# Kernel tuning notes

Measured on AMD Instinct MI355X. Metric: run time of the kernel, lower is better.

## Reference

```python
import jax, jax.numpy as jnp
import numpy as np

B, L, C = 2, 2048, 2048
H, HKV, D = 16, 4, 128  # heads, kv heads, head_dim
G = H // HKV            # GQA group size
NEG = -1e9


def rms_norm(x, w, eps=1e-6):
    # FastRMSNorm: compute in fp32, scale by weight, cast back
    xf = x.astype(jnp.float32)
    y = xf * jax.lax.rsqrt(jnp.mean(xf * xf, axis=-1, keepdims=True) + eps) * w
    return y.astype(x.dtype)


def apply_rope(t, cos, sin):
    # t: (B, h, L, D); cos/sin: (L, D//2) broadcast to (1,1,L,D//2)
    t1, t2 = jnp.split(t, 2, axis=-1)
    c = cos[None, None]
    s = sin[None, None]
    return jnp.concatenate([t1 * c - t2 * s, t2 * c + t1 * s], axis=-1)


def setup_inputs() -> dict:
    key = jax.random.key(0)
    ks = jax.random.split(key, 8)
    x = jax.random.normal(ks[0], (B, L, C), jnp.float32)
    Wq = jax.random.normal(ks[1], (H * D, C), jnp.float32) * 0.02
    Wk = jax.random.normal(ks[2], (HKV * D, C), jnp.float32) * 0.02
    Wv = jax.random.normal(ks[3], (HKV * D, C), jnp.float32) * 0.02
    Wo = jax.random.normal(ks[4], (C, H * D), jnp.float32) * 0.02
    q_norm_w = jnp.ones((D,), jnp.float32)
    k_norm_w = jnp.ones((D,), jnp.float32)
    pos = jnp.arange(L, dtype=jnp.float32)[:, None]
    inv_freq = 1.0 / (10000.0 ** (jnp.arange(0, D, 2, dtype=jnp.float32) / D))
    ang = pos * inv_freq[None, :]            # (L, D//2)
    rope_cos = jnp.cos(ang)
    rope_sin = jnp.sin(ang)
    # VAR-style block-causal visibility: 8 blocks of 256, query block i sees key blocks <= i
    blk = jnp.arange(L) // 256
    vis = blk[None, :] <= blk[:, None]       # (L, L) bool
    attn_bias = jnp.where(vis, 0.0, NEG).astype(jnp.float32)[None, None]  # (1,1,L,L)
    return dict(x=x, Wq=Wq, Wk=Wk, Wv=Wv, Wo=Wo, q_norm_w=q_norm_w,
                k_norm_w=k_norm_w, rope_cos=rope_cos, rope_sin=rope_sin,
                attn_bias=attn_bias)


def reference(x, Wq, Wk, Wv, Wo, q_norm_w, k_norm_w, rope_cos, rope_sin, attn_bias):
    b, l, c = x.shape
    # fused projections -> (B, h, L, D)
    q = rms_norm((x @ Wq.T).reshape(b, l, H, D), q_norm_w).transpose(0, 2, 1, 3)
    k = rms_norm((x @ Wk.T).reshape(b, l, HKV, D), k_norm_w).transpose(0, 2, 1, 3)
    v = (x @ Wv.T).reshape(b, l, HKV, D).transpose(0, 2, 1, 3)
    q = apply_rope(q, rope_cos, rope_sin)
    k = apply_rope(k, rope_cos, rope_sin)
    scale = D ** -0.5
    # GQA: group query heads over kv heads
    qg = q.reshape(b, HKV, G, l, D)
    scores = jnp.einsum('bkgqd,bkKd->bkgqK', qg, k) * scale
    scores = scores + attn_bias[:, :, None]  # broadcast (1,1,1,L,L)
    probs = jax.nn.softmax(scores, axis=-1)
    out = jnp.einsum('bkgqK,bkKd->bkgqd', probs, v)
    out = out.reshape(b, H, l, D).transpose(0, 2, 1, 3).reshape(b, l, H * D)
    return out @ Wo.T
```

## Files before the change

### kernel.cpp

```cpp
#include <hip/hip_runtime.h>

#define B_ 2
#define L_ 2048
#define C_ 2048
#define H_ 16
#define HKV_ 4
#define D_ 128
#define G_ (H_ / HKV_)
#define TOK_ (B_ * L_)
#define NQKV_ 3072

typedef __bf16 bf16;
typedef __bf16 bf16x4 __attribute__((ext_vector_type(4)));
typedef __bf16 bf16x8 __attribute__((ext_vector_type(8)));
typedef float f32x4 __attribute__((ext_vector_type(4)));

__device__ inline void gload16(const void* g, void* l) {
  __builtin_amdgcn_global_load_lds(
      (const __attribute__((address_space(1))) void*)g,
      (__attribute__((address_space(3))) void*)l, 16, 0, 0);
}

#define N4_X  2097152
#define N4_WQ 1048576
#define N4_WK 262144
#define N4_WV 262144
#define N4_WO 1048576
#define N4_TOT (N4_X + N4_WQ + N4_WK + N4_WV + N4_WO)

__global__ void cvt_all(const float* __restrict__ x, const float* __restrict__ wq,
                        const float* __restrict__ wk, const float* __restrict__ wv,
                        const float* __restrict__ wo, bf16* __restrict__ dst) {
  int stride = gridDim.x * blockDim.x;
  for (int j = blockIdx.x * blockDim.x + threadIdx.x; j < N4_TOT; j += stride) {
    const float* s;
    int off;
    if (j < N4_X) { s = x; off = j; }
    else if (j < N4_X + N4_WQ) { s = wq; off = j - N4_X; }
    else if (j < N4_X + N4_WQ + N4_WK) { s = wk; off = j - (N4_X + N4_WQ); }
    else if (j < N4_X + N4_WQ + N4_WK + N4_WV) { s = wv; off = j - (N4_X + N4_WQ + N4_WK); }
    else { s = wo; off = j - (N4_X + N4_WQ + N4_WK + N4_WV); }
    float4 v = reinterpret_cast<const float4*>(s)[off];
    bf16x4 o = {(bf16)v.x, (bf16)v.y, (bf16)v.z, (bf16)v.w};
    reinterpret_cast<bf16x4*>(dst)[j] = o;
  }
}

template <bool OUT_F32>
__global__ __launch_bounds__(256, 3) void gemm_bt(
    const bf16* __restrict__ A, const bf16* __restrict__ Bm,
    void* __restrict__ Cm, int M, int N, int K) {
  __shared__ __align__(16) bf16 sA[3][128 * 32];
  __shared__ __align__(16) bf16 sB[3][128 * 32];
  const int tid = threadIdx.x;
  const int row0 = blockIdx.x * 128, col0 = blockIdx.y * 128;
  const int wid = tid >> 6, lane = tid & 63;
  const int wr = wid >> 1, wc = wid & 1;
  const int l15 = lane & 15, kk = (lane >> 4) * 8;
  f32x4 acc[4][4] = {};
  const int nk = K / 32;
  const int r0 = tid >> 2, c0 = tid & 3;
  const int r1 = 64 + r0, c1 = c0;
  const int ldsA0 = (wid * 64) * 8, ldsA1 = (256 + wid * 64) * 8;

  auto stage = [&](int kt, int slot) {
    gload16(A + (size_t)(row0 + r0) * K + kt * 32 + c0 * 8, &sA[slot][ldsA0]);
    gload16(A + (size_t)(row0 + r1) * K + kt * 32 + c1 * 8, &sA[slot][ldsA1]);
    gload16(Bm + (size_t)(col0 + r0) * K + kt * 32 + c0 * 8, &sB[slot][ldsA0]);
    gload16(Bm + (size_t)(col0 + r1) * K + kt * 32 + c1 * 8, &sB[slot][ldsA1]);
  };

  stage(0, 0);
  stage(1, 1);
  asm volatile("s_waitcnt vmcnt(4)" ::: "memory");
  __builtin_amdgcn_s_barrier();
  __builtin_amdgcn_sched_barrier(0);

  int slot = 0;
  for (int kt = 0; kt < nk; ++kt) {
    int s2 = slot + 2; if (s2 >= 3) s2 -= 3;
    if (kt + 2 < nk) stage(kt + 2, s2);
    const bf16* cA = sA[slot];
    const bf16* cB = sB[slot];
    bf16x8 af[4], bfr[4];
#pragma unroll
    for (int m = 0; m < 4; ++m)
      af[m] = *reinterpret_cast<const bf16x8*>(cA + (wr * 64 + m * 16 + l15) * 32 + kk);
#pragma unroll
    for (int n = 0; n < 4; ++n)
      bfr[n] = *reinterpret_cast<const bf16x8*>(cB + (wc * 64 + n * 16 + l15) * 32 + kk);
    __builtin_amdgcn_s_setprio(1);
#pragma unroll
    for (int m = 0; m < 4; ++m)
#pragma unroll
      for (int n = 0; n < 4; ++n)
        acc[m][n] = __builtin_amdgcn_mfma_f32_16x16x32_bf16(af[m], bfr[n], acc[m][n], 0, 0, 0);
    __builtin_amdgcn_s_setprio(0);
    if (kt + 2 < nk)
      asm volatile("s_waitcnt vmcnt(4)" ::: "memory");
    else
      asm volatile("s_waitcnt vmcnt(0)" ::: "memory");
    __builtin_amdgcn_s_barrier();
    __builtin_amdgcn_sched_barrier(0);
    slot = (slot + 1 == 3) ? 0 : slot + 1;
  }
#pragma unroll
  for (int m = 0; m < 4; ++m)
#pragma unroll
    for (int n = 0; n < 4; ++n)
#pragma unroll
      for (int r = 0; r < 4; ++r) {
        int row = row0 + wr * 64 + m * 16 + (lane >> 4) * 4 + r;
        int col = col0 + wc * 64 + n * 16 + l15;
        if constexpr (OUT_F32)
          reinterpret_cast<float*>(Cm)[(size_t)row * N + col] = acc[m][n][r];
        else
          reinterpret_cast<bf16*>(Cm)[(size_t)row * N + col] = (bf16)acc[m][n][r];
      }
}

__global__ void k_norm_rope(const bf16* __restrict__ proj,
                            const float* __restrict__ normw,
                            const float* __restrict__ cosb,
                            const float* __restrict__ sinb,
                            bf16* __restrict__ out) {
  int wid = (blockIdx.x * blockDim.x + threadIdx.x) >> 6;
  int lane = threadIdx.x & 63;
  int head = wid & 3, tok = wid >> 2;
  int b = tok / L_, l = tok % L_;
  const bf16* p = proj + (size_t)tok * NQKV_ + H_ * D_ + head * D_;
  float t1 = (float)p[lane];
  float t2 = (float)p[lane + 64];
  float ss = t1 * t1 + t2 * t2;
#pragma unroll
  for (int off = 32; off; off >>= 1) ss += __shfl_xor(ss, off);
  float r = rsqrtf(ss * (1.0f / 128.0f) + 1e-6f);
  float n1 = t1 * r * normw[lane];
  float n2 = t2 * r * normw[lane + 64];
  float c = cosb[l * 64 + lane], s = sinb[l * 64 + lane];
  bf16* q = out + (((size_t)b * HKV_ + head) * L_ + l) * D_;
  q[lane] = (bf16)(n1 * c - n2 * s);
  q[lane + 64] = (bf16)(n2 * c + n1 * s);
}

__global__ __launch_bounds__(256) void v_transpose(const bf16* __restrict__ proj,
                                                   bf16* __restrict__ vt) {
  __shared__ __align__(16) bf16 sT[64 * 136];
  const int t = threadIdx.x;
  const int l0 = blockIdx.x * 64;
  const int bk = blockIdx.y;
  const bf16* src = proj + (size_t)((bk >> 2) * L_ + l0) * NQKV_ + (H_ + HKV_) * D_ + (bk & 3) * D_;
#pragma unroll
  for (int c = 0; c < 4; ++c) {
    int idx = c * 256 + t;
    int l = idx >> 4, dc = idx & 15;
    bf16x8 v = *reinterpret_cast<const bf16x8*>(src + (size_t)l * NQKV_ + dc * 8);
    *reinterpret_cast<bf16x8*>((char*)sT + l * 272 + ((dc ^ (l >> 3)) << 4)) = v;
  }
  __syncthreads();
  bf16* dst = vt + (size_t)bk * D_ * L_ + l0;
#pragma unroll
  for (int c = 0; c < 4; ++c) {
    int idx = c * 256 + t;
    int d = idx >> 3, lg = idx & 7;
    bf16x8 o;
#pragma unroll
    for (int j = 0; j < 8; ++j) {
      int l = lg * 8 + j;
      o[j] = *reinterpret_cast<const bf16*>((char*)sT + l * 272 + (((d >> 3) ^ lg) << 4) + (d & 7) * 2);
    }
    *reinterpret_cast<bf16x8*>(dst + (size_t)d * L_ + lg * 8) = o;
  }
}

#define SM_K0 0
#define SM_K1 16384
#define SM_V0 32768
#define SM_V1 49152
#define SM_P  65536
__global__ __launch_bounds__(512, 4) void attn_fused(
    const bf16* __restrict__ QKV,
    const bf16* __restrict__ Kn,
    const bf16* __restrict__ Vt,
    const float* __restrict__ qnw,
    const float* __restrict__ cosb, const float* __restrict__ sinb,
    bf16* __restrict__ AO) {
  __shared__ __align__(16) char smem[81920];
  const int tid = threadIdx.x;
  const int wid = tid >> 6, lane = tid & 63;
  const int bid = blockIdx.x;
  const int bk = bid & 7;
  const int qt = (bid < 256) ? (bid >> 3) : 63 - ((bid - 256) >> 3);
  const int b = bk >> 2;
  const int hl = wid & 3, qs = wid >> 2;
  const int h = (bk & 3) * G_ + hl;
  const int qrow0 = qt * 32 + qs * 16;
  const int l15 = lane & 15, g4 = lane >> 4, kk = g4 * 8;
  const int swz = (l15 & 7) << 4;

  const int qrow = qrow0 + l15;
  const bf16* qsrc = QKV + (size_t)(b * L_ + qrow) * NQKV_ + h * D_;
  float t[4][8];
  float ss = 0.f;
#pragma unroll
  for (int c = 0; c < 4; ++c) {
    bf16x8 v = *reinterpret_cast<const bf16x8*>(qsrc + c * 32 + kk);
#pragma unroll
    for (int j = 0; j < 8; ++j) { t[c][j] = (float)v[j]; ss += t[c][j] * t[c][j]; }
  }

  const int kr0 = tid >> 4, kc0 = tid & 15;
  const int kr1 = 32 + kr0;
  const int vr0 = tid >> 3, vc0 = tid & 7;
  const int vr1 = 64 + vr0;
  const bf16* kb = Kn + (size_t)bk * L_ * D_;
  const bf16* vb = Vt + (size_t)bk * D_ * (size_t)L_;
  const bf16* kp0 = kb + (size_t)kr0 * D_ + ((kc0 ^ (kr0 & 7)) * 8);
  const bf16* kp1 = kb + (size_t)kr1 * D_ + ((kc0 ^ (kr1 & 7)) * 8);
  const bf16* vp0 = vb + (size_t)vr0 * L_ + ((vc0 ^ (vr0 & 7)) * 8);
  const bf16* vp1 = vb + (size_t)vr1 * L_ + ((vc0 ^ (vr1 & 7)) * 8);

  const int ntiles = ((qt >> 3) + 1) * 4;
  gload16(kp0, smem + SM_K0 + tid * 16);
  gload16(kp1, smem + SM_K0 + 8192 + tid * 16);
  gload16(vp0, smem + SM_V0 + tid * 16);
  gload16(vp1, smem + SM_V0 + 8192 + tid * 16);

  constexpr float SCL = 0.12752650038632816f;
  ss += __shfl_xor(ss, 16);
  ss += __shfl_xor(ss, 32);
  const float rr = rsqrtf(ss * (1.0f / 128.0f) + 1e-6f);
  bf16x8 qf[4];
#pragma unroll
  for (int c = 0; c < 2; ++c)
#pragma unroll
    for (int j = 0; j < 8; ++j) {
      int i = c * 32 + kk + j;
      float n1 = t[c][j] * rr * qnw[i];
      float n2 = t[c + 2][j] * rr * qnw[i + 64];
      float cs = cosb[qrow * 64 + i], sn = sinb[qrow * 64 + i];
      qf[c][j] = (bf16)((n1 * cs - n2 * sn) * SCL);
      qf[c + 2][j] = (bf16)((n2 * cs + n1 * sn) * SCL);
    }

  int aK[4], aV[2], aPw[4];
#pragma unroll
  for (int c = 0; c < 4; ++c)
    aK[c] = l15 * 256 + ((((c << 2) + g4) ^ (l15 & 7)) << 4);
#pragma unroll
  for (int hh = 0; hh < 2; ++hh)
    aV[hh] = l15 * 128 + ((((hh << 2) + g4) ^ (l15 & 7)) << 4);
  const int pbase = SM_P + wid * 2048 + l15 * 128;
#pragma unroll
  for (int n = 0; n < 4; ++n)
    aPw[n] = pbase + (((n << 5) + (g4 << 3)) ^ swz);
  const int aPr0 = pbase + ((g4 << 4) ^ swz);
  const int aPr1 = pbase + ((64 + (g4 << 4)) ^ swz);

  f32x4 acc[8] = {};
  float mref = -1e30f, lpart = 0.f;

  __syncthreads();

  auto tile_step = [&](int KB, int VB, int KBn, int VBn, int ktNext, bool doPref) {
    if (doPref) {
      gload16(kp0 + (size_t)ktNext * 64 * D_, smem + KBn + tid * 16);
      gload16(kp1 + (size_t)ktNext * 64 * D_, smem + KBn + 8192 + tid * 16);
      gload16(vp0 + ktNext * 64, smem + VBn + tid * 16);
      gload16(vp1 + ktNext * 64, smem + VBn + 8192 + tid * 16);
    }
    f32x4 s[4];
    __builtin_amdgcn_s_setprio(1);
#pragma unroll
    for (int n = 0; n < 4; ++n) {
      f32x4 st = {};
#pragma unroll
      for (int c = 0; c < 4; ++c) {
        bf16x8 kf = *reinterpret_cast<const bf16x8*>(smem + KB + n * 4096 + aK[c]);
        st = __builtin_amdgcn_mfma_f32_16x16x32_bf16(kf, qf[c], st, 0, 0, 0);
      }
      s[n] = st;
    }
    __builtin_amdgcn_s_setprio(0);
    float pm = fmaxf(fmaxf(s[0][0], s[0][1]), fmaxf(s[0][2], s[0][3]));
#pragma unroll
    for (int n = 1; n < 4; ++n)
      pm = fmaxf(pm, fmaxf(fmaxf(s[n][0], s[n][1]), fmaxf(s[n][2], s[n][3])));
    if (!__all(pm <= mref + 8.f)) {
      pm = fmaxf(pm, __shfl_xor(pm, 16));
      pm = fmaxf(pm, __shfl_xor(pm, 32));
      float mnew = fmaxf(mref, pm);
      float resc = exp2f(mref - mnew);
      mref = mnew;
      lpart *= resc;
#pragma unroll
      for (int f = 0; f < 8; ++f) acc[f] *= resc;
    }
    float qsum[4];
#pragma unroll
    for (int n = 0; n < 4; ++n) {
      float p0 = exp2f(s[n][0] - mref);
      float p1 = exp2f(s[n][1] - mref);
      float p2 = exp2f(s[n][2] - mref);
      float p3 = exp2f(s[n][3] - mref);
      bf16x4 pw = {(bf16)p0, (bf16)p1, (bf16)p2, (bf16)p3};
      *reinterpret_cast<bf16x4*>(smem + aPw[n]) = pw;
      qsum[n] = (p0 + p1) + (p2 + p3);
    }
    lpart += (qsum[0] + qsum[1]) + (qsum[2] + qsum[3]);
    bf16x8 pf0 = *reinterpret_cast<const bf16x8*>(smem + aPr0);
    bf16x8 pf1 = *reinterpret_cast<const bf16x8*>(smem + aPr1);
    __builtin_amdgcn_s_setprio(1);
#pragma unroll
    for (int f = 0; f < 8; ++f) {
      bf16x8 vf0 = *reinterpret_cast<const bf16x8*>(smem + VB + f * 2048 + aV[0]);
      acc[f] = __builtin_amdgcn_mfma_f32_16x16x32_bf16(vf0, pf0, acc[f], 0, 0, 0);
      bf16x8 vf1 = *reinterpret_cast<const bf16x8*>(smem + VB + f * 2048 + aV[1]);
      acc[f] = __builtin_amdgcn_mfma_f32_16x16x32_bf16(vf1, pf1, acc[f], 0, 0, 0);
    }
    __builtin_amdgcn_s_setprio(0);
    __syncthreads();
  };

  for (int kt = 0; kt < ntiles; kt += 2) {
    tile_step(SM_K0, SM_V0, SM_K1, SM_V1, kt + 1, true);
    tile_step(SM_K1, SM_V1, SM_K0, SM_V0, kt + 2, kt + 2 < ntiles);
  }

  lpart += __shfl_xor(lpart, 16);
  lpart += __shfl_xor(lpart, 32);
  const float rinv = 1.f / lpart;
  bf16* aop = AO + ((size_t)(b * L_ + qrow0 + l15) * H_ + h) * D_ + (g4 << 2);
#pragma unroll
  for (int f = 0; f < 8; ++f) {
    bf16x4 o = {(bf16)(acc[f][0] * rinv), (bf16)(acc[f][1] * rinv),
                (bf16)(acc[f][2] * rinv), (bf16)(acc[f][3] * rinv)};
    *reinterpret_cast<bf16x4*>(aop + f * 16) = o;
  }
}

extern "C" void kernel_launch(void* const* d_in, const int* in_sizes, int n_in,
                              void* d_out, int out_size, void* d_ws, size_t ws_size,
                              hipStream_t stream) {
  const float* x = (const float*)d_in[0];
  const float* Wq = (const float*)d_in[1];
  const float* Wk = (const float*)d_in[2];
  const float* Wv = (const float*)d_in[3];
  const float* Wo = (const float*)d_in[4];
  const float* qnw = (const float*)d_in[5];
  const float* knw = (const float*)d_in[6];
  const float* rc = (const float*)d_in[7];
  const float* rs = (const float*)d_in[8];
  float* out = (float*)d_out;

  char* ws = (char*)d_ws;
  bf16* xb = (bf16*)ws;    ws += (size_t)TOK_ * C_ * 2;
  bf16* wqb = (bf16*)ws;   ws += (size_t)(H_ * D_) * C_ * 2;
  bf16* wkb = (bf16*)ws;   ws += (size_t)(HKV_ * D_) * C_ * 2;
  bf16* wvb = (bf16*)ws;   ws += (size_t)(HKV_ * D_) * C_ * 2;
  bf16* wob = (bf16*)ws;   ws += (size_t)C_ * (H_ * D_) * 2;
  bf16* qkv = (bf16*)ws;   ws += (size_t)TOK_ * NQKV_ * 2;
  bf16* Kb = (bf16*)ws;    ws += (size_t)TOK_ * HKV_ * D_ * 2;
  bf16* Vtb = (bf16*)ws;   ws += (size_t)TOK_ * HKV_ * D_ * 2;
  bf16* AOb = xb;

  cvt_all<<<2048, 256, 0, stream>>>(x, Wq, Wk, Wv, Wo, xb);

  gemm_bt<false><<<dim3(TOK_ / 128, NQKV_ / 128), 256, 0, stream>>>(
      xb, wqb, qkv, TOK_, NQKV_, C_);

  k_norm_rope<<<(TOK_ * HKV_) / 4, 256, 0, stream>>>(qkv, knw, rc, rs, Kb);
  v_transpose<<<dim3(L_ / 64, B_ * HKV_), 256, 0, stream>>>(qkv, Vtb);

  attn_fused<<<512, 512, 0, stream>>>(qkv, Kb, Vtb, qnw, rc, rs, AOb);

  gemm_bt<true><<<dim3(TOK_ / 128, C_ / 128), 256, 0, stream>>>(
      AOb, wob, out, TOK_, C_, H_ * D_);
}
```

Measured before the change: 201.9 us.

## Use three-stage 32-key K/V pipeline with explicit vmcnt waits in attention

The attention kernel now streams K/V in 32-key tiles through a triple-buffered LDS ring, prefetching two tiles ahead, instead of 64-key tiles double-buffered one ahead. Synchronisation becomes explicit s_waitcnt vmcnt plus s_barrier in place of __syncthreads, and the P scratch shrinks, cutting LDS from 80KB to 56KB. The aim is deeper latency hiding and lower LDS use per block, which may raise occupancy. The cost is twice as many barriers and softmax max/rescale checks per key, and smaller MFMA batches per iteration.

Measured after the change: 209.9 us. 4.0% more time.

```diff
diff --git a/kernel.cpp b/kernel.cpp
--- a/kernel.cpp
+++ b/kernel.cpp
@@ -173,11 +173,8 @@
   }
 }
 
-#define SM_K0 0
-#define SM_K1 16384
-#define SM_V0 32768
-#define SM_V1 49152
-#define SM_P  65536
+#define SM_V  24576
+#define SM_P  49152
 __global__ __launch_bounds__(512, 4) void attn_fused(
     const bf16* __restrict__ QKV,
     const bf16* __restrict__ Kn,
@@ -185,7 +182,7 @@
     const float* __restrict__ qnw,
     const float* __restrict__ cosb, const float* __restrict__ sinb,
     bf16* __restrict__ AO) {
-  __shared__ __align__(16) char smem[81920];
+  __shared__ __align__(16) char smem[57344];
   const int tid = threadIdx.x;
   const int wid = tid >> 6, lane = tid & 63;
   const int bid = blockIdx.x;
@@ -196,7 +193,23 @@
   const int h = (bk & 3) * G_ + hl;
   const int qrow0 = qt * 32 + qs * 16;
   const int l15 = lane & 15, g4 = lane >> 4, kk = g4 * 8;
-  const int swz = (l15 & 7) << 4;
+
+  const int kr = tid >> 4, kc = tid & 15;
+  const int vr = tid >> 2, vc = tid & 3;
+  const bf16* kb = Kn + (size_t)bk * L_ * D_;
+  const bf16* vb = Vt + (size_t)bk * D_ * (size_t)L_;
+  const bf16* kp = kb + (size_t)kr * D_ + ((kc ^ (kr & 7)) * 8);
+  const bf16* vp = vb + (size_t)vr * L_ + ((vc ^ (vr & 3)) * 8);
+
+  const int ntiles = ((qt >> 3) + 1) * 8;
+
+  auto stage = [&](int kt, int slot) {
+    gload16(kp + (size_t)kt * 32 * D_, smem + slot * 8192 + tid * 16);
+    gload16(vp + kt * 32, smem + SM_V + slot * 8192 + tid * 16);
+  };
+
+  stage(0, 0);
+  stage(1, 1);
 
   const int qrow = qrow0 + l15;
   const bf16* qsrc = QKV + (size_t)(b * L_ + qrow) * NQKV_ + h * D_;
@@ -208,24 +221,6 @@
 #pragma unroll
     for (int j = 0; j < 8; ++j) { t[c][j] = (float)v[j]; ss += t[c][j] * t[c][j]; }
   }
-
-  const int kr0 = tid >> 4, kc0 = tid & 15;
-  const int kr1 = 32 + kr0;
-  const int vr0 = tid >> 3, vc0 = tid & 7;
-  const int vr1 = 64 + vr0;
-  const bf16* kb = Kn + (size_t)bk * L_ * D_;
-  const bf16* vb = Vt + (size_t)bk * D_ * (size_t)L_;
-  const bf16* kp0 = kb + (size_t)kr0 * D_ + ((kc0 ^ (kr0 & 7)) * 8);
-  const bf16* kp1 = kb + (size_t)kr1 * D_ + ((kc0 ^ (kr1 & 7)) * 8);
-  const bf16* vp0 = vb + (size_t)vr0 * L_ + ((vc0 ^ (vr0 & 7)) * 8);
-  const bf16* vp1 = vb + (size_t)vr1 * L_ + ((vc0 ^ (vr1 & 7)) * 8);
-
-  const int ntiles = ((qt >> 3) + 1) * 4;
-  gload16(kp0, smem + SM_K0 + tid * 16);
-  gload16(kp1, smem + SM_K0 + 8192 + tid * 16);
-  gload16(vp0, smem + SM_V0 + tid * 16);
-  gload16(vp1, smem + SM_V0 + 8192 + tid * 16);
-
   constexpr float SCL = 0.12752650038632816f;
   ss += __shfl_xor(ss, 16);
   ss += __shfl_xor(ss, 32);
@@ -243,49 +238,42 @@
       qf[c + 2][j] = (bf16)((n2 * cs + n1 * sn) * SCL);
     }
 
-  int aK[4], aV[2], aPw[4];
+  int aK[4];
 #pragma unroll
   for (int c = 0; c < 4; ++c)
     aK[c] = l15 * 256 + ((((c << 2) + g4) ^ (l15 & 7)) << 4);
-#pragma unroll
-  for (int hh = 0; hh < 2; ++hh)
-    aV[hh] = l15 * 128 + ((((hh << 2) + g4) ^ (l15 & 7)) << 4);
-  const int pbase = SM_P + wid * 2048 + l15 * 128;
-#pragma unroll
-  for (int n = 0; n < 4; ++n)
-    aPw[n] = pbase + (((n << 5) + (g4 << 3)) ^ swz);
-  const int aPr0 = pbase + ((g4 << 4) ^ swz);
-  const int aPr1 = pbase + ((64 + (g4 << 4)) ^ swz);
+  const int aV = l15 * 64 + ((g4 ^ (l15 & 3)) << 4);
+  const int swz64 = (l15 & 3) << 4;
+  const int pbase = SM_P + wid * 1024 + l15 * 64;
+  const int aPw0 = pbase + ((g4 << 3) ^ swz64);
+  const int aPw1 = pbase + ((32 + (g4 << 3)) ^ swz64);
+  const int aPr = pbase + ((g4 << 4) ^ swz64);
 
   f32x4 acc[8] = {};
   float mref = -1e30f, lpart = 0.f;
 
-  __syncthreads();
-
-  auto tile_step = [&](int KB, int VB, int KBn, int VBn, int ktNext, bool doPref) {
-    if (doPref) {
-      gload16(kp0 + (size_t)ktNext * 64 * D_, smem + KBn + tid * 16);
-      gload16(kp1 + (size_t)ktNext * 64 * D_, smem + KBn + 8192 + tid * 16);
-      gload16(vp0 + ktNext * 64, smem + VBn + tid * 16);
-      gload16(vp1 + ktNext * 64, smem + VBn + 8192 + tid * 16);
-    }
-    f32x4 s[4];
+  asm volatile("s_waitcnt vmcnt(2)" ::: "memory");
+  __builtin_amdgcn_s_barrier();
+  __builtin_amdgcn_sched_barrier(0);
+
+  int slot = 0;
+  for (int kt = 0; kt < ntiles; ++kt) {
+    int s2 = slot + 2; if (s2 >= 3) s2 -= 3;
+    if (kt + 2 < ntiles) stage(kt + 2, s2);
+    const int kbase = slot * 8192;
+    const int vbase = SM_V + slot * 8192;
+    f32x4 s0 = {}, s1 = {};
     __builtin_amdgcn_s_setprio(1);
 #pragma unroll
-    for (int n = 0; n < 4; ++n) {
-      f32x4 st = {};
-#pragma unroll
-      for (int c = 0; c < 4; ++c) {
-        bf16x8 kf = *reinterpret_cast<const bf16x8*>(smem + KB + n * 4096 + aK[c]);
-        st = __builtin_amdgcn_mfma_f32_16x16x32_bf16(kf, qf[c], st, 0, 0, 0);
-      }
-      s[n] = st;
+    for (int c = 0; c < 4; ++c) {
+      bf16x8 kf0 = *reinterpret_cast<const bf16x8*>(smem + kbase + aK[c]);
+      s0 = __builtin_amdgcn_mfma_f32_16x16x32_bf16(kf0, qf[c], s0, 0, 0, 0);
+      bf16x8 kf1 = *reinterpret_cast<const bf16x8*>(smem + kbase + 4096 + aK[c]);
+      s1 = __builtin_amdgcn_mfma_f32_16x16x32_bf16(kf1, qf[c], s1, 0, 0, 0);
     }
     __builtin_amdgcn_s_setprio(0);
-    float pm = fmaxf(fmaxf(s[0][0], s[0][1]), fmaxf(s[0][2], s[0][3]));
-#pragma unroll
-    for (int n = 1; n < 4; ++n)
-      pm = fmaxf(pm, fmaxf(fmaxf(s[n][0], s[n][1]), fmaxf(s[n][2], s[n][3])));
+    float pm = fmaxf(fmaxf(fmaxf(s0[0], s0[1]), fmaxf(s0[2], s0[3])),
+                     fmaxf(fmaxf(s1[0], s1[1]), fmaxf(s1[2], s1[3])));
     if (!__all(pm <= mref + 8.f)) {
       pm = fmaxf(pm, __shfl_xor(pm, 16));
       pm = fmaxf(pm, __shfl_xor(pm, 32));
@@ -296,35 +284,32 @@
 #pragma unroll
       for (int f = 0; f < 8; ++f) acc[f] *= resc;
     }
-    float qsum[4];
-#pragma unroll
-    for (int n = 0; n < 4; ++n) {
-      float p0 = exp2f(s[n][0] - mref);
-      float p1 = exp2f(s[n][1] - mref);
-      float p2 = exp2f(s[n][2] - mref);
-      float p3 = exp2f(s[n][3] - mref);
-      bf16x4 pw = {(bf16)p0, (bf16)p1, (bf16)p2, (bf16)p3};
-      *reinterpret_cast<bf16x4*>(smem + aPw[n]) = pw;
-      qsum[n] = (p0 + p1) + (p2 + p3);
-    }
-    lpart += (qsum[0] + qsum[1]) + (qsum[2] + qsum[3]);
-    bf16x8 pf0 = *reinterpret_cast<const bf16x8*>(smem + aPr0);
-    bf16x8 pf1 = *reinterpret_cast<const bf16x8*>(smem + aPr1);
+    {
+      float p0 = exp2f(s0[0] - mref), p1 = exp2f(s0[1] - mref);
+      float p2 = exp2f(s0[2] - mref), p3 = exp2f(s0[3] - mref);
+      bf16x4 w0 = {(bf16)p0, (bf16)p1, (bf16)p2, (bf16)p3};
+      *reinterpret_cast<bf16x4*>(smem + aPw0) = w0;
+      float p4 = exp2f(s1[0] - mref), p5 = exp2f(s1[1] - mref);
+      float p6 = exp2f(s1[2] - mref), p7 = exp2f(s1[3] - mref);
+      bf16x4 w1 = {(bf16)p4, (bf16)p5, (bf16)p6, (bf16)p7};
+      *reinterpret_cast<bf16x4*>(smem + aPw1) = w1;
+      lpart += ((p0 + p1) + (p2 + p3)) + ((p4 + p5) + (p6 + p7));
+    }
+    bf16x8 pf = *reinterpret_cast<const bf16x8*>(smem + aPr);
     __builtin_amdgcn_s_setprio(1);
 #pragma unroll
     for (int f = 0; f < 8; ++f) {
-      bf16x8 vf0 = *reinterpret_cast<const bf16x8*>(smem + VB + f * 2048 + aV[0]);
-      acc[f] = __builtin_amdgcn_mfma_f32_16x16x32_bf16(vf0, pf0, acc[f], 0, 0, 0);
-      bf16x8 vf1 = *reinterpret_cast<const bf16x8*>(smem + VB + f * 2048 + aV[1]);
-      acc[f] = __builtin_amdgcn_mfma_f32_16x16x32_bf16(vf1, pf1, acc[f], 0, 0, 0);
+      bf16x8 vf = *reinterpret_cast<const bf16x8*>(smem + vbase + f * 1024 + aV);
+      acc[f] = __builtin_amdgcn_mfma_f32_16x16x32_bf16(vf, pf, acc[f], 0, 0, 0);
     }
     __builtin_amdgcn_s_setprio(0);
-    __syncthreads();
-  };
-
-  for (int kt = 0; kt < ntiles; kt += 2) {
-    tile_step(SM_K0, SM_V0, SM_K1, SM_V1, kt + 1, true);
-    tile_step(SM_K1, SM_V1, SM_K0, SM_V0, kt + 2, kt + 2 < ntiles);
+    if (kt + 2 < ntiles)
+      asm volatile("s_waitcnt vmcnt(2)" ::: "memory");
+    else
+      asm volatile("s_waitcnt vmcnt(0)" ::: "memory");
+    __builtin_amdgcn_s_barrier();
+    __builtin_amdgcn_sched_barrier(0);
+    slot = (slot + 1 == 3) ? 0 : slot + 1;
   }
 
   lpart += __shfl_xor(lpart, 16);
```

## Software-pipeline QK^T one tile ahead of softmax and PV in attention loop

Applied to the files above, without the earlier changes.

Restructures the attention inner loop so the QK^T MFMAs for tile kt+1 are issued before the softmax and PV of tile kt. K is now prefetched two tiles ahead and V one tile ahead, and the first two K tiles are loaded in the prologue. The aim is to overlap exp/softmax VALU work with matrix-core work and hide LDS latency. In exchange it holds an extra set of score registers, which may raise VGPR pressure and lower occupancy, and the buffer rotation is more intricate.

After: 222.7 us. 10.3% more time.

```diff
diff --git a/kernel.cpp b/kernel.cpp
--- a/kernel.cpp
+++ b/kernel.cpp
@@ -225,6 +225,8 @@
   gload16(kp1, smem + SM_K0 + 8192 + tid * 16);
   gload16(vp0, smem + SM_V0 + tid * 16);
   gload16(vp1, smem + SM_V0 + 8192 + tid * 16);
+  gload16(kp0 + (size_t)64 * D_, smem + SM_K1 + tid * 16);
+  gload16(kp1 + (size_t)64 * D_, smem + SM_K1 + 8192 + tid * 16);
 
   constexpr float SCL = 0.12752650038632816f;
   ss += __shfl_xor(ss, 16);
@@ -259,17 +261,9 @@
 
   f32x4 acc[8] = {};
   float mref = -1e30f, lpart = 0.f;
-
-  __syncthreads();
-
-  auto tile_step = [&](int KB, int VB, int KBn, int VBn, int ktNext, bool doPref) {
-    if (doPref) {
-      gload16(kp0 + (size_t)ktNext * 64 * D_, smem + KBn + tid * 16);
-      gload16(kp1 + (size_t)ktNext * 64 * D_, smem + KBn + 8192 + tid * 16);
-      gload16(vp0 + ktNext * 64, smem + VBn + tid * 16);
-      gload16(vp1 + ktNext * 64, smem + VBn + 8192 + tid * 16);
-    }
-    f32x4 s[4];
+  f32x4 scur[4];
+
+  auto qkt = [&](int KB, f32x4* sout) {
     __builtin_amdgcn_s_setprio(1);
 #pragma unroll
     for (int n = 0; n < 4; ++n) {
@@ -279,13 +273,32 @@
         bf16x8 kf = *reinterpret_cast<const bf16x8*>(smem + KB + n * 4096 + aK[c]);
         st = __builtin_amdgcn_mfma_f32_16x16x32_bf16(kf, qf[c], st, 0, 0, 0);
       }
-      s[n] = st;
+      sout[n] = st;
     }
     __builtin_amdgcn_s_setprio(0);
-    float pm = fmaxf(fmaxf(s[0][0], s[0][1]), fmaxf(s[0][2], s[0][3]));
+  };
+
+  __syncthreads();
+  qkt(SM_K0, scur);
+  __syncthreads();
+
+  auto step = [&](int KB_qkt, int KB_st, int VB_cur, int VB_st, int kt) {
+    const bool doK = kt + 2 < ntiles;
+    const bool doV = kt + 1 < ntiles;
+    if (doK) {
+      gload16(kp0 + (size_t)(kt + 2) * 64 * D_, smem + KB_st + tid * 16);
+      gload16(kp1 + (size_t)(kt + 2) * 64 * D_, smem + KB_st + 8192 + tid * 16);
+    }
+    if (doV) {
+      gload16(vp0 + (kt + 1) * 64, smem + VB_st + tid * 16);
+      gload16(vp1 + (kt + 1) * 64, smem + VB_st + 8192 + tid * 16);
+    }
+    f32x4 snxt[4];
+    if (doV) qkt(KB_qkt, snxt);
+    float pm = fmaxf(fmaxf(scur[0][0], scur[0][1]), fmaxf(scur[0][2], scur[0][3]));
 #pragma unroll
     for (int n = 1; n < 4; ++n)
-      pm = fmaxf(pm, fmaxf(fmaxf(s[n][0], s[n][1]), fmaxf(s[n][2], s[n][3])));
+      pm = fmaxf(pm, fmaxf(fmaxf(scur[n][0], scur[n][1]), fmaxf(scur[n][2], scur[n][3])));
     if (!__all(pm <= mref + 8.f)) {
       pm = fmaxf(pm, __shfl_xor(pm, 16));
       pm = fmaxf(pm, __shfl_xor(pm, 32));
@@ -299,10 +312,10 @@
     float qsum[4];
 #pragma unroll
     for (int n = 0; n < 4; ++n) {
-      float p0 = exp2f(s[n][0] - mref);
-      float p1 = exp2f(s[n][1] - mref);
-      float p2 = exp2f(s[n][2] - mref);
-      float p3 = exp2f(s[n][3] - mref);
+      float p0 = exp2f(scur[n][0] - mref);
+      float p1 = exp2f(scur[n][1] - mref);
+      float p2 = exp2f(scur[n][2] - mref);
+      float p3 = exp2f(scur[n][3] - mref);
       bf16x4 pw = {(bf16)p0, (bf16)p1, (bf16)p2, (bf16)p3};
       *reinterpret_cast<bf16x4*>(smem + aPw[n]) = pw;
       qsum[n] = (p0 + p1) + (p2 + p3);
@@ -313,18 +326,22 @@
     __builtin_amdgcn_s_setprio(1);
 #pragma unroll
     for (int f = 0; f < 8; ++f) {
-      bf16x8 vf0 = *reinterpret_cast<const bf16x8*>(smem + VB + f * 2048 + aV[0]);
+      bf16x8 vf0 = *reinterpret_cast<const bf16x8*>(smem + VB_cur + f * 2048 + aV[0]);
       acc[f] = __builtin_amdgcn_mfma_f32_16x16x32_bf16(vf0, pf0, acc[f], 0, 0, 0);
-      bf16x8 vf1 = *reinterpret_cast<const bf16x8*>(smem + VB + f * 2048 + aV[1]);
+      bf16x8 vf1 = *reinterpret_cast<const bf16x8*>(smem + VB_cur + f * 2048 + aV[1]);
       acc[f] = __builtin_amdgcn_mfma_f32_16x16x32_bf16(vf1, pf1, acc[f], 0, 0, 0);
     }
     __builtin_amdgcn_s_setprio(0);
     __syncthreads();
+    if (doV) {
+#pragma unroll
+      for (int n = 0; n < 4; ++n) scur[n] = snxt[n];
+    }
   };
 
   for (int kt = 0; kt < ntiles; kt += 2) {
-    tile_step(SM_K0, SM_V0, SM_K1, SM_V1, kt + 1, true);
-    tile_step(SM_K1, SM_V1, SM_K0, SM_V0, kt + 2, kt + 2 < ntiles);
+    step(SM_K1, SM_K0, SM_V0, SM_V1, kt);
+    step(SM_K0, SM_K1, SM_V1, SM_V0, kt + 1);
   }
 
   lpart += __shfl_xor(lpart, 16);
```
